# Kernel tuning notes

Measured on AMD Instinct MI355X. Metric: run time of the kernel, lower is better.

## Reference

```python
import jax, jax.numpy as jnp
import numpy as np

D_MODEL, D_FF, H, B, S = 1024, 4096, 16, 4, 2048
D_K = D_MODEL // H
EPS = 1e-5
NEG = -1e9


def _custom_ln(x, alpha, bias):
    # torch: mean, std (unbiased, N-1), alpha*(x-mean)/(std+eps)+bias; alpha/bias scalars
    mean = jnp.mean(x, axis=-1, keepdims=True)
    n = x.shape[-1]
    var = jnp.sum((x - mean) ** 2, axis=-1, keepdims=True) / (n - 1)
    std = jnp.sqrt(var)
    return alpha * (x - mean) / (std + EPS) + bias


def setup_inputs() -> dict:
    key = jax.random.key(0)
    ks = jax.random.split(key, 12)
    sc_d = 1.0 / np.sqrt(D_MODEL)
    sc_f = 1.0 / np.sqrt(D_FF)
    inp = {
        "x": jax.random.normal(ks[0], (B, S, D_MODEL), jnp.float32),
        "src_mask": jnp.ones((B, 1, 1, S), jnp.int32),
        "wq": jax.random.normal(ks[1], (D_MODEL, D_MODEL), jnp.float32) * sc_d,
        "bq": jnp.zeros((D_MODEL,), jnp.float32),
        "wk": jax.random.normal(ks[2], (D_MODEL, D_MODEL), jnp.float32) * sc_d,
        "bk": jnp.zeros((D_MODEL,), jnp.float32),
        "wv": jax.random.normal(ks[3], (D_MODEL, D_MODEL), jnp.float32) * sc_d,
        "bv": jnp.zeros((D_MODEL,), jnp.float32),
        "wo": jax.random.normal(ks[4], (D_MODEL, D_MODEL), jnp.float32) * sc_d,
        "bo": jnp.zeros((D_MODEL,), jnp.float32),
        "w1": jax.random.normal(ks[5], (D_MODEL, D_FF), jnp.float32) * sc_d,
        "b1": jnp.zeros((D_FF,), jnp.float32),
        "w2": jax.random.normal(ks[6], (D_FF, D_MODEL), jnp.float32) * sc_f,
        "b2": jnp.zeros((D_MODEL,), jnp.float32),
        "ln1_a": jnp.ones((1,), jnp.float32),
        "ln1_b": jnp.zeros((1,), jnp.float32),
        "ln2_a": jnp.ones((1,), jnp.float32),
        "ln2_b": jnp.zeros((1,), jnp.float32),
    }
    return inp


def _attention(xn, src_mask, wq, bq, wk, bk, wv, bv, wo, bo):
    q = (xn @ wq + bq).reshape(B, S, H, D_K).transpose(0, 2, 1, 3)  # [B,H,S,Dk]
    k = (xn @ wk + bk).reshape(B, S, H, D_K).transpose(0, 2, 1, 3)
    v = (xn @ wv + bv).reshape(B, S, H, D_K).transpose(0, 2, 1, 3)
    scores = jnp.einsum("bhqd,bhkd->bhqk", q, k) / np.sqrt(D_K)
    scores = jnp.where(src_mask == 0, NEG, scores)
    attn = jax.nn.softmax(scores, axis=-1)
    ctx = jnp.einsum("bhqk,bhkd->bhqd", attn, v)
    ctx = ctx.transpose(0, 2, 1, 3).reshape(B, S, D_MODEL)
    return ctx @ wo + bo


def reference(x, src_mask, wq, bq, wk, bk, wv, bv, wo, bo,
              w1, b1, w2, b2, ln1_a, ln1_b, ln2_a, ln2_b):
    # pre-LN attention residual (dropout=0 -> identity)
    xn = _custom_ln(x, ln1_a, ln1_b)
    x = x + _attention(xn, src_mask, wq, bq, wk, bk, wv, bv, wo, bo)
    # pre-LN FFN residual
    xn = _custom_ln(x, ln2_a, ln2_b)
    ff = jax.nn.relu(xn @ w1 + b1) @ w2 + b2
    return x + ff
```

## Files before the change

kernel.cpp:

```cpp
#include <hip/hip_runtime.h>

typedef unsigned short u16;
typedef __bf16 bf16x8 __attribute__((ext_vector_type(8)));
typedef float f32x4 __attribute__((ext_vector_type(4)));

__device__ __forceinline__ u16 f2bf(float f) {
  unsigned u = __builtin_bit_cast(unsigned, f);
  unsigned lsb = (u >> 16) & 1u;
  u += 0x7fffu + lsb;
  return (u16)(u >> 16);
}

__device__ __forceinline__ unsigned cvt_pk_bf16(float lo, float hi) {
  unsigned r;
  asm("v_cvt_pk_bf16_f32 %0, %1, %2" : "=v"(r) : "v"(lo), "v"(hi));
  return r;
}

__device__ __forceinline__ void gld_lds16(const u16* g, u16* l) {
  __builtin_amdgcn_global_load_lds(
      (__attribute__((address_space(1))) void*)g,
      (__attribute__((address_space(3))) void*)l, 16, 0, 0);
}

__global__ __launch_bounds__(256) void ln_kernel(
    const float* __restrict__ x, u16* __restrict__ out,
    const float* __restrict__ alpha_p, const float* __restrict__ beta_p) {
  const int row = blockIdx.x;
  const int t = threadIdx.x;
  const float4 v = reinterpret_cast<const float4*>(x + (size_t)row * 1024)[t];
  float s = v.x + v.y + v.z + v.w;
  float sq = v.x * v.x + v.y * v.y + v.z * v.z + v.w * v.w;
#pragma unroll
  for (int off = 32; off > 0; off >>= 1) {
    s += __shfl_down(s, off);
    sq += __shfl_down(sq, off);
  }
  __shared__ float red[8];
  const int w = t >> 6;
  if ((t & 63) == 0) { red[w] = s; red[4 + w] = sq; }
  __syncthreads();
  const float ts = red[0] + red[1] + red[2] + red[3];
  const float tq = red[4] + red[5] + red[6] + red[7];
  const float mean = ts * (1.0f / 1024.0f);
  float var = (tq - ts * mean) * (1.0f / 1023.0f);
  var = fmaxf(var, 0.0f);
  const float rden = 1.0f / (sqrtf(var) + 1e-5f);
  const float a = alpha_p[0], bb = beta_p[0];
  uint2 ov;
  ov.x = cvt_pk_bf16(a * (v.x - mean) * rden + bb, a * (v.y - mean) * rden + bb);
  ov.y = cvt_pk_bf16(a * (v.z - mean) * rden + bb, a * (v.w - mean) * rden + bb);
  reinterpret_cast<uint2*>(out + (size_t)row * 1024)[t] = ov;
}

__global__ __launch_bounds__(256) void wcvt_t(
    const float* __restrict__ w, u16* __restrict__ wt, int K, int N, float scale) {
  __shared__ float tile[32][33];
  const int n0 = blockIdx.x * 32, k0 = blockIdx.y * 32;
  const int tx = threadIdx.x, ty = threadIdx.y;
#pragma unroll
  for (int i = 0; i < 4; ++i)
    tile[ty + i * 8][tx] = w[(size_t)(k0 + ty + i * 8) * N + n0 + tx];
  __syncthreads();
#pragma unroll
  for (int i = 0; i < 4; ++i)
    wt[(size_t)(n0 + ty + i * 8) * K + k0 + tx] = f2bf(tile[tx][ty + i * 8] * scale);
}

__global__ __launch_bounds__(256) void pack_bias(
    const float* __restrict__ a, const float* __restrict__ b,
    const float* __restrict__ c, float* __restrict__ o, float qscale) {
  const int i = blockIdx.x * 256 + threadIdx.x;
  o[i] = (i < 1024) ? a[i] * qscale : ((i < 2048) ? b[i - 1024] : c[i - 2048]);
}

__global__ __launch_bounds__(256) void mk_mbias(
    const int* __restrict__ mask, float* __restrict__ mb, int* __restrict__ flags) {
  const int b = blockIdx.x, t = threadIdx.x;
  __shared__ int bad;
  if (t == 0) bad = 0;
  __syncthreads();
  int loc = 0;
#pragma unroll
  for (int i = 0; i < 8; ++i) {
    const int idx = b * 2048 + t * 8 + i;
    const int mv = mask[idx];
    mb[idx] = mv ? 0.f : -1.4427e9f;
    loc |= (mv == 0);
  }
  if (loc) atomicOr(&bad, 1);
  __syncthreads();
  if (t == 0) flags[b] = !bad;
}

template <int EPI, int BM>
__global__ __launch_bounds__(512, BM == 256 ? 2 : 4) void gemm8(
    const u16* __restrict__ A, const u16* __restrict__ Bt,
    const float* __restrict__ bias, const float* __restrict__ res,
    void* __restrict__ Cout, u16* __restrict__ vt, int M, int N, int K) {
  constexpr int MF = BM / 32;
  constexpr int NA = (BM == 256) ? 2 : 1;
  extern __shared__ u16 smem[];
  u16* Asb = smem;
  u16* Bsb = smem + 3 * BM * 32;

  const int tid = threadIdx.x;
  const int l = tid & 63;
  const int w = tid >> 6;
  const int wr = w >> 2, wc = w & 3;
  const int gx = gridDim.x;
  int id = blockIdx.y * gx + blockIdx.x;
  const int nwg = gx * gridDim.y;
  id = (id & 7) * (nwg >> 3) + (id >> 3);
  const int n0 = (id % gx) * 256;
  const int m0 = (id / gx) * BM;
  const int lr = l & 15, lg = l >> 4;
  const int koff = (lg ^ ((lr >> 1) & 3)) * 8;

  f32x4 acc[MF][4];
#pragma unroll
  for (int i = 0; i < MF; ++i)
#pragma unroll
    for (int j = 0; j < 4; ++j) acc[i][j] = f32x4{0.f, 0.f, 0.f, 0.f};

  const u16* aSrc[NA];
  int aOff[NA];
#pragma unroll
  for (int i = 0; i < NA; ++i) {
    const int ci = tid + i * 512;
    const int row = ci >> 2, c = ci & 3;
    const int sc = c ^ ((row >> 1) & 3);
    aSrc[i] = A + (size_t)(m0 + row) * K + sc * 8;
    aOff[i] = ci * 8;
  }
  const u16* bSrc[2];
  int bOff[2];
#pragma unroll
  for (int i = 0; i < 2; ++i) {
    const int ci = tid + i * 512;
    const int row = ci >> 2, c = ci & 3;
    const int sc = c ^ ((row >> 1) & 3);
    bSrc[i] = Bt + (size_t)(n0 + row) * K + sc * 8;
    bOff[i] = ci * 8;
  }

  const int NT = K >> 5;
#pragma unroll
  for (int i = 0; i < NA; ++i) gld_lds16(aSrc[i], Asb + aOff[i]);
#pragma unroll
  for (int i = 0; i < 2; ++i) gld_lds16(bSrc[i], Bsb + bOff[i]);
#pragma unroll
  for (int i = 0; i < NA; ++i) gld_lds16(aSrc[i] + 32, Asb + BM * 32 + aOff[i]);
#pragma unroll
  for (int i = 0; i < 2; ++i) gld_lds16(bSrc[i] + 32, Bsb + 256 * 32 + bOff[i]);
  if constexpr (NA == 2) asm volatile("s_waitcnt vmcnt(4)" ::: "memory");
  else asm volatile("s_waitcnt vmcnt(3)" ::: "memory");
  __builtin_amdgcn_s_barrier();

  int cur = 0;
  for (int t = 0; t < NT; ++t) {
    const int nx2 = (cur + 2 >= 3) ? cur - 1 : cur + 2;
    if (t + 2 < NT) {
      const int ko = (t + 2) * 32;
#pragma unroll
      for (int i = 0; i < NA; ++i) gld_lds16(aSrc[i] + ko, Asb + nx2 * BM * 32 + aOff[i]);
#pragma unroll
      for (int i = 0; i < 2; ++i) gld_lds16(bSrc[i] + ko, Bsb + nx2 * 256 * 32 + bOff[i]);
    }
    const u16* Ab = Asb + cur * BM * 32;
    const u16* Bb = Bsb + cur * 256 * 32;
    bf16x8 a[MF], b[4];
#pragma unroll
    for (int mf = 0; mf < MF; ++mf)
      a[mf] = *reinterpret_cast<const bf16x8*>(&Ab[(wr * (BM / 2) + mf * 16 + lr) * 32 + koff]);
#pragma unroll
    for (int nf = 0; nf < 4; ++nf)
      b[nf] = *reinterpret_cast<const bf16x8*>(&Bb[(wc * 64 + nf * 16 + lr) * 32 + koff]);
    __builtin_amdgcn_s_setprio(1);
#pragma unroll
    for (int mf = 0; mf < MF; ++mf)
#pragma unroll
      for (int nf = 0; nf < 4; ++nf)
        acc[mf][nf] = __builtin_amdgcn_mfma_f32_16x16x32_bf16(a[mf], b[nf], acc[mf][nf], 0, 0, 0);
    __builtin_amdgcn_s_setprio(0);
    if (t + 2 < NT) {
      if constexpr (NA == 2) asm volatile("s_waitcnt vmcnt(4)" ::: "memory");
      else asm volatile("s_waitcnt vmcnt(3)" ::: "memory");
    } else {
      asm volatile("s_waitcnt vmcnt(0)" ::: "memory");
    }
    __builtin_amdgcn_s_barrier();
    cur = (cur + 1 >= 3) ? 0 : cur + 1;
  }

  if (EPI == 3 && n0 >= 2048) {
#pragma unroll
    for (int mf = 0; mf < MF; ++mf) {
#pragma unroll
      for (int nf = 0; nf < 4; ++nf) {
        const int col = n0 + wc * 64 + nf * 16 + lr;
        const float bv = bias[col];
        const int row0 = m0 + wr * (BM / 2) + mf * 16 + lg * 4;
        const int bb = row0 >> 11, s0 = row0 & 2047;
        const int d = col - 2048;
        uint2 pv;
        pv.x = cvt_pk_bf16(acc[mf][nf][0] + bv, acc[mf][nf][1] + bv);
        pv.y = cvt_pk_bf16(acc[mf][nf][2] + bv, acc[mf][nf][3] + bv);
        *reinterpret_cast<uint2*>(vt + ((size_t)bb * 1024 + d) * 2048 + s0) = pv;
      }
    }
    return;
  }

#pragma unroll
  for (int mf = 0; mf < MF; ++mf) {
#pragma unroll
    for (int nf = 0; nf < 4; ++nf) {
      const int col = n0 + wc * 64 + nf * 16 + lr;
      const float bv = bias[col];
#pragma unroll
      for (int j = 0; j < 4; ++j) {
        const int row = m0 + wr * (BM / 2) + mf * 16 + lg * 4 + j;
        const size_t idx = (size_t)row * N + col;
        const float vv = acc[mf][nf][j] + bv;
        if (EPI == 1)
          ((float*)Cout)[idx] = vv + res[idx];
        else if (EPI == 2)
          ((u16*)Cout)[idx] = f2bf(fmaxf(vv, 0.f));
        else
          ((u16*)Cout)[idx] = f2bf(vv);
      }
    }
  }
}

__global__ __launch_bounds__(256, 4) void attn_fwd7(
    const u16* __restrict__ qkv, const u16* __restrict__ vt,
    const float* __restrict__ mbias, const int* __restrict__ flags,
    u16* __restrict__ ctx) {
  __shared__ u16 Ks[2][64 * 64];
  __shared__ u16 Vs[2][64 * 64];
  const int tid = threadIdx.x;
  const int l = tid & 63;
  const int w = tid >> 6;
  const int p = blockIdx.y * 16 + blockIdx.x;
  const int idx = p >> 3;
  const int bh = (p & 7) * 8 + (idx >> 4);
  const int qx = idx & 15;
  const int b = bh >> 4, h = bh & 15;
  const int r0 = qx * 128 + w * 32;
  const int lr = l & 15, lg = l >> 4;

  const u16* qb = qkv + (size_t)b * 2048 * 3072 + h * 64;
  const u16* kp = qb + 1024;
  const u16* vb = vt + ((size_t)b * 1024 + h * 64) * 2048;
  const float* mb = mbias + (size_t)b * 2048;
  const int allLive = flags[b];

  bf16x8 qf[2][2];
#pragma unroll
  for (int m = 0; m < 2; ++m)
#pragma unroll
    for (int ks = 0; ks < 2; ++ks)
      qf[m][ks] = *reinterpret_cast<const bf16x8*>(
          qb + (size_t)(r0 + m * 16 + lr) * 3072 + ks * 32 + lg * 8);

  bf16x8 ones;
#pragma unroll
  for (int e = 0; e < 8; ++e) ones[e] = (__bf16)1.0f;

  float mrun[2] = {-1e30f, -1e30f};
  f32x4 osum[2];
  f32x4 o[2][4];
#pragma unroll
  for (int m = 0; m < 2; ++m) {
    osum[m] = f32x4{0.f, 0.f, 0.f, 0.f};
#pragma unroll
    for (int d = 0; d < 4; ++d) o[m][d] = f32x4{0.f, 0.f, 0.f, 0.f};
  }

  const u16* kS[2];
  const u16* vS[2];
#pragma unroll
  for (int i = 0; i < 2; ++i) {
    const int ci = tid + i * 256;
    const int row = ci >> 3, cc = ci & 7;
    const int sc = cc ^ (row & 7);
    kS[i] = kp + (size_t)row * 3072 + sc * 8;
    vS[i] = vb + (size_t)row * 2048 + sc * 8;
  }
#pragma unroll
  for (int i = 0; i < 2; ++i) {
    const int ci8 = (tid + i * 256) * 8;
    gld_lds16(kS[i], &Ks[0][ci8]);
    gld_lds16(vS[i], &Vs[0][ci8]);
  }
  asm volatile("s_waitcnt vmcnt(0)" ::: "memory");
  __syncthreads();

  union U8 { unsigned u[4]; bf16x8 v; };

  int cur = 0;
  for (int t = 0; t < 32; ++t) {
    const int kb0 = t * 64;
    if (t + 1 < 32) {
      const int nb = kb0 + 64;
#pragma unroll
      for (int i = 0; i < 2; ++i) {
        const int ci8 = (tid + i * 256) * 8;
        gld_lds16(kS[i] + (size_t)nb * 3072, &Ks[cur ^ 1][ci8]);
        gld_lds16(vS[i] + nb, &Vs[cur ^ 1][ci8]);
      }
    }

    f32x4 st[2][4];
    __builtin_amdgcn_s_setprio(1);
#pragma unroll
    for (int cf = 0; cf < 4; ++cf) {
      const int krow = cf * 16 + lr;
      const int ch0 = lg ^ (krow & 7);
      const int ch1 = (4 + lg) ^ (krow & 7);
      const bf16x8 kf0 = *reinterpret_cast<const bf16x8*>(&Ks[cur][krow * 64 + ch0 * 8]);
      const bf16x8 kf1 = *reinterpret_cast<const bf16x8*>(&Ks[cur][krow * 64 + ch1 * 8]);
#pragma unroll
      for (int m = 0; m < 2; ++m) {
        f32x4 acc = __builtin_amdgcn_mfma_f32_16x16x32_bf16(kf0, qf[m][0],
                                                            f32x4{0.f, 0.f, 0.f, 0.f}, 0, 0, 0);
        st[m][cf] = __builtin_amdgcn_mfma_f32_16x16x32_bf16(kf1, qf[m][1], acc, 0, 0, 0);
      }
    }
    __builtin_amdgcn_s_setprio(0);

    if (!allLive) {
#pragma unroll
      for (int cf = 0; cf < 4; ++cf) {
        const float4 m4 = *reinterpret_cast<const float4*>(mb + kb0 + cf * 16 + lg * 4);
#pragma unroll
        for (int m = 0; m < 2; ++m) {
          st[m][cf][0] += m4.x;
          st[m][cf][1] += m4.y;
          st[m][cf][2] += m4.z;
          st[m][cf][3] += m4.w;
        }
      }
    }

    bf16x8 paA[2], paB[2];
#pragma unroll
    for (int m = 0; m < 2; ++m) {
      float p0 = fmaxf(fmaxf(st[m][0][0], st[m][0][1]), st[m][0][2]);
      float p1 = fmaxf(fmaxf(st[m][0][3], st[m][1][0]), st[m][1][1]);
      float p2 = fmaxf(fmaxf(st[m][1][2], st[m][1][3]), st[m][2][0]);
      float p3 = fmaxf(fmaxf(st[m][2][1], st[m][2][2]), st[m][2][3]);
      float p4 = fmaxf(fmaxf(st[m][3][0], st[m][3][1]), st[m][3][2]);
      float pm = fmaxf(fmaxf(p0, p1), p2);
      pm = fmaxf(fmaxf(pm, p3), p4);
      pm = fmaxf(pm, st[m][3][3]);
      pm = fmaxf(pm, __shfl_xor(pm, 16));
      pm = fmaxf(pm, __shfl_xor(pm, 32));
      if (__any(pm > mrun[m] + 8.f)) {
        const float mn = fmaxf(mrun[m], pm);
        const float corr = exp2f(mrun[m] - mn);
        mrun[m] = mn;
#pragma unroll
        for (int j = 0; j < 4; ++j) osum[m][j] *= corr;
#pragma unroll
        for (int d = 0; d < 4; ++d)
#pragma unroll
          for (int j = 0; j < 4; ++j) o[m][d][j] *= corr;
      }
#pragma unroll
      for (int cf = 0; cf < 4; ++cf)
#pragma unroll
        for (int j = 0; j < 4; ++j)
          st[m][cf][j] = exp2f(st[m][cf][j] - mrun[m]);

      unsigned pk[4][2];
#pragma unroll
      for (int cf = 0; cf < 4; ++cf)
#pragma unroll
        for (int wp = 0; wp < 2; ++wp)
          pk[cf][wp] = cvt_pk_bf16(st[m][cf][2 * wp], st[m][cf][2 * wp + 1]);

      U8 a0, a1;
#pragma unroll
      for (int c = 0; c < 2; ++c) {
        const int src = lr + 16 * ((2 * lg + c) & 3);
#pragma unroll
        for (int wp = 0; wp < 2; ++wp) {
          const int v00 = __shfl((int)pk[0][wp], src);
          const int v01 = __shfl((int)pk[1][wp], src);
          const int v10 = __shfl((int)pk[2][wp], src);
          const int v11 = __shfl((int)pk[3][wp], src);
          a0.u[2 * c + wp] = (unsigned)((lg < 2) ? v00 : v01);
          a1.u[2 * c + wp] = (unsigned)((lg < 2) ? v10 : v11);
        }
      }
      paA[m] = a0.v;
      paB[m] = a1.v;
    }

    __builtin_amdgcn_s_setprio(1);
#pragma unroll
    for (int df = 0; df < 4; ++df) {
      const int vrow = df * 16 + lr;
      const int ch0 = lg ^ (vrow & 7);
      const int ch1 = (4 + lg) ^ (vrow & 7);
      const bf16x8 vf0 = *reinterpret_cast<const bf16x8*>(&Vs[cur][vrow * 64 + ch0 * 8]);
      const bf16x8 vf1 = *reinterpret_cast<const bf16x8*>(&Vs[cur][vrow * 64 + ch1 * 8]);
#pragma unroll
      for (int m = 0; m < 2; ++m) {
        o[m][df] = __builtin_amdgcn_mfma_f32_16x16x32_bf16(vf0, paA[m], o[m][df], 0, 0, 0);
        o[m][df] = __builtin_amdgcn_mfma_f32_16x16x32_bf16(vf1, paB[m], o[m][df], 0, 0, 0);
      }
    }
#pragma unroll
    for (int m = 0; m < 2; ++m) {
      osum[m] = __builtin_amdgcn_mfma_f32_16x16x32_bf16(ones, paA[m], osum[m], 0, 0, 0);
      osum[m] = __builtin_amdgcn_mfma_f32_16x16x32_bf16(ones, paB[m], osum[m], 0, 0, 0);
    }
    __builtin_amdgcn_s_setprio(0);

    asm volatile("s_waitcnt vmcnt(0)" ::: "memory");
    __syncthreads();
    cur ^= 1;
  }

#pragma unroll
  for (int m = 0; m < 2; ++m) {
    const float rdiv = 1.f / osum[m][0];
    const size_t rowbase = ((size_t)b * 2048 + r0 + m * 16 + lr) * 1024 + h * 64;
#pragma unroll
    for (int df = 0; df < 4; ++df) {
      uint2 s4;
      s4.x = cvt_pk_bf16(o[m][df][0] * rdiv, o[m][df][1] * rdiv);
      s4.y = cvt_pk_bf16(o[m][df][2] * rdiv, o[m][df][3] * rdiv);
      *reinterpret_cast<uint2*>(ctx + rowbase + df * 16 + lg * 4) = s4;
    }
  }
}

extern "C" void kernel_launch(void* const* d_in, const int* in_sizes, int n_in,
                              void* d_out, int out_size, void* d_ws, size_t ws_size,
                              hipStream_t stream) {
  const float* x = (const float*)d_in[0];
  const int* mask = (const int*)d_in[1];
  const float* wq = (const float*)d_in[2];
  const float* bq = (const float*)d_in[3];
  const float* wk = (const float*)d_in[4];
  const float* bk = (const float*)d_in[5];
  const float* wv = (const float*)d_in[6];
  const float* bv = (const float*)d_in[7];
  const float* wo = (const float*)d_in[8];
  const float* bo = (const float*)d_in[9];
  const float* w1 = (const float*)d_in[10];
  const float* b1 = (const float*)d_in[11];
  const float* w2 = (const float*)d_in[12];
  const float* b2 = (const float*)d_in[13];
  const float* ln1a = (const float*)d_in[14];
  const float* ln1b = (const float*)d_in[15];
  const float* ln2a = (const float*)d_in[16];
  const float* ln2b = (const float*)d_in[17];

  const float SCL2 = 0.125f * 1.4426950408889634f;
  const size_t LDS256 = 3 * (256 + 256) * 32 * sizeof(u16);
  const size_t LDS128 = 3 * (128 + 256) * 32 * sizeof(u16);

  hipFuncSetAttribute((const void*)&gemm8<3, 256>,
                      hipFuncAttributeMaxDynamicSharedMemorySize, (int)LDS256);
  hipFuncSetAttribute((const void*)&gemm8<2, 256>,
                      hipFuncAttributeMaxDynamicSharedMemorySize, (int)LDS256);
  hipFuncSetAttribute((const void*)&gemm8<1, 128>,
                      hipFuncAttributeMaxDynamicSharedMemorySize, (int)LDS128);

  char* ws = (char*)d_ws;
  const size_t MB = 1024ull * 1024ull;
  u16* WTQKV = (u16*)(ws + 0 * MB);
  u16* WTO = (u16*)(ws + 6 * MB);
  u16* W1T = (u16*)(ws + 8 * MB);
  u16* W2T = (u16*)(ws + 16 * MB);
  float* BQKV = (float*)(ws + 24 * MB);
  float* MBIAS = (float*)(ws + 24 * MB + 65536);
  int* FLAGS = (int*)(ws + 24 * MB + 131072);
  u16* QKV = (u16*)(ws + 25 * MB);
  u16* VT = (u16*)(ws + 73 * MB);
  u16* XN = (u16*)(ws + 89 * MB);
  u16* CTX = (u16*)(ws + 105 * MB);
  float* X2 = (float*)(ws + 25 * MB);
  u16* XN2 = (u16*)(ws + 57 * MB);
  u16* H1 = (u16*)(ws + 73 * MB);

  dim3 bt(32, 8);
  wcvt_t<<<dim3(32, 32), bt, 0, stream>>>(wq, WTQKV, 1024, 1024, SCL2);
  wcvt_t<<<dim3(32, 32), bt, 0, stream>>>(wk, WTQKV + 1024 * 1024, 1024, 1024, 1.f);
  wcvt_t<<<dim3(32, 32), bt, 0, stream>>>(wv, WTQKV + 2048 * 1024, 1024, 1024, 1.f);
  wcvt_t<<<dim3(32, 32), bt, 0, stream>>>(wo, WTO, 1024, 1024, 1.f);
  wcvt_t<<<dim3(128, 32), bt, 0, stream>>>(w1, W1T, 1024, 4096, 1.f);
  wcvt_t<<<dim3(32, 128), bt, 0, stream>>>(w2, W2T, 4096, 1024, 1.f);
  pack_bias<<<dim3(12), 256, 0, stream>>>(bq, bk, bv, BQKV, SCL2);
  mk_mbias<<<dim3(4), 256, 0, stream>>>(mask, MBIAS, FLAGS);

  ln_kernel<<<8192, 256, 0, stream>>>(x, XN, ln1a, ln1b);
  gemm8<3, 256><<<dim3(12, 32), 512, LDS256, stream>>>(XN, WTQKV, BQKV, nullptr, QKV, VT, 8192, 3072, 1024);
  attn_fwd7<<<dim3(16, 64), 256, 0, stream>>>(QKV, VT, MBIAS, FLAGS, CTX);
  gemm8<1, 128><<<dim3(4, 64), 512, LDS128, stream>>>(CTX, WTO, bo, x, X2, nullptr, 8192, 1024, 1024);
  ln_kernel<<<8192, 256, 0, stream>>>(X2, XN2, ln2a, ln2b);
  gemm8<2, 256><<<dim3(16, 32), 512, LDS256, stream>>>(XN2, W1T, b1, nullptr, H1, nullptr, 8192, 4096, 1024);
  gemm8<1, 128><<<dim3(4, 64), 512, LDS128, stream>>>(H1, W2T, b2, X2, (float*)d_out, nullptr, 8192, 1024, 4096);
}
```

Baseline: 455.4 us.

## Triple-buffer attention K/V tiles with one barrier per iteration

The attention kernel moves from double to triple-buffered K/V LDS tiles, prefetching two tiles ahead. It uses a partial vmcnt wait and a single barrier at the top of each iteration instead of a full drain plus barrier at the end. It also swaps __shfl for ds_bpermute with precomputed byte offsets. The larger LDS footprint lowers the occupancy hint from 4 to 3 blocks per CU, trading latency hiding from occupancy for latency hiding from deeper prefetch.

```diff
diff --git a/kernel.cpp b/kernel.cpp
--- a/kernel.cpp
+++ b/kernel.cpp
@@ -234,12 +234,12 @@
   }
 }
 
-__global__ __launch_bounds__(256, 4) void attn_fwd7(
+__global__ __launch_bounds__(256, 3) void attn_fwd8(
     const u16* __restrict__ qkv, const u16* __restrict__ vt,
     const float* __restrict__ mbias, const int* __restrict__ flags,
     u16* __restrict__ ctx) {
-  __shared__ u16 Ks[2][64 * 64];
-  __shared__ u16 Vs[2][64 * 64];
+  __shared__ u16 Ks[3][64 * 64];
+  __shared__ u16 Vs[3][64 * 64];
   const int tid = threadIdx.x;
   const int l = tid & 63;
   const int w = tid >> 6;
@@ -279,6 +279,9 @@
     for (int d = 0; d < 4; ++d) o[m][d] = f32x4{0.f, 0.f, 0.f, 0.f};
   }
 
+  const int srcb0 = (lr + 16 * ((2 * lg + 0) & 3)) << 2;
+  const int srcb1 = (lr + 16 * ((2 * lg + 1) & 3)) << 2;
+
   const u16* kS[2];
   const u16* vS[2];
 #pragma unroll
@@ -295,23 +298,31 @@
     gld_lds16(kS[i], &Ks[0][ci8]);
     gld_lds16(vS[i], &Vs[0][ci8]);
   }
-  asm volatile("s_waitcnt vmcnt(0)" ::: "memory");
-  __syncthreads();
+#pragma unroll
+  for (int i = 0; i < 2; ++i) {
+    const int ci8 = (tid + i * 256) * 8;
+    gld_lds16(kS[i] + (size_t)64 * 3072, &Ks[1][ci8]);
+    gld_lds16(vS[i] + 64, &Vs[1][ci8]);
+  }
 
   union U8 { unsigned u[4]; bf16x8 v; };
 
   int cur = 0;
   for (int t = 0; t < 32; ++t) {
-    const int kb0 = t * 64;
-    if (t + 1 < 32) {
-      const int nb = kb0 + 64;
+    if (t < 31) asm volatile("s_waitcnt vmcnt(4)" ::: "memory");
+    else asm volatile("s_waitcnt vmcnt(0)" ::: "memory");
+    __builtin_amdgcn_s_barrier();
+    if (t + 2 < 32) {
+      const int nx2 = (cur + 2 >= 3) ? cur - 1 : cur + 2;
+      const int nb = (t + 2) * 64;
 #pragma unroll
       for (int i = 0; i < 2; ++i) {
         const int ci8 = (tid + i * 256) * 8;
-        gld_lds16(kS[i] + (size_t)nb * 3072, &Ks[cur ^ 1][ci8]);
-        gld_lds16(vS[i] + nb, &Vs[cur ^ 1][ci8]);
-      }
-    }
+        gld_lds16(kS[i] + (size_t)nb * 3072, &Ks[nx2][ci8]);
+        gld_lds16(vS[i] + nb, &Vs[nx2][ci8]);
+      }
+    }
+    const int kb0 = t * 64;
 
     f32x4 st[2][4];
     __builtin_amdgcn_s_setprio(1);
@@ -385,13 +396,13 @@
       U8 a0, a1;
 #pragma unroll
       for (int c = 0; c < 2; ++c) {
-        const int src = lr + 16 * ((2 * lg + c) & 3);
+        const int srcb = c ? srcb1 : srcb0;
 #pragma unroll
         for (int wp = 0; wp < 2; ++wp) {
-          const int v00 = __shfl((int)pk[0][wp], src);
-          const int v01 = __shfl((int)pk[1][wp], src);
-          const int v10 = __shfl((int)pk[2][wp], src);
-          const int v11 = __shfl((int)pk[3][wp], src);
+          const int v00 = __builtin_amdgcn_ds_bpermute(srcb, (int)pk[0][wp]);
+          const int v01 = __builtin_amdgcn_ds_bpermute(srcb, (int)pk[1][wp]);
+          const int v10 = __builtin_amdgcn_ds_bpermute(srcb, (int)pk[2][wp]);
+          const int v11 = __builtin_amdgcn_ds_bpermute(srcb, (int)pk[3][wp]);
           a0.u[2 * c + wp] = (unsigned)((lg < 2) ? v00 : v01);
           a1.u[2 * c + wp] = (unsigned)((lg < 2) ? v10 : v11);
         }
@@ -421,9 +432,7 @@
     }
     __builtin_amdgcn_s_setprio(0);
 
-    asm volatile("s_waitcnt vmcnt(0)" ::: "memory");
-    __syncthreads();
-    cur ^= 1;
+    cur = (cur + 1 >= 3) ? 0 : cur + 1;
   }
 
 #pragma unroll
@@ -502,7 +511,7 @@
 
   ln_kernel<<<8192, 256, 0, stream>>>(x, XN, ln1a, ln1b);
   gemm8<3, 256><<<dim3(12, 32), 512, LDS256, stream>>>(XN, WTQKV, BQKV, nullptr, QKV, VT, 8192, 3072, 1024);
-  attn_fwd7<<<dim3(16, 64), 256, 0, stream>>>(QKV, VT, MBIAS, FLAGS, CTX);
+  attn_fwd8<<<dim3(16, 64), 256, 0, stream>>>(QKV, VT, MBIAS, FLAGS, CTX);
   gemm8<1, 128><<<dim3(4, 64), 512, LDS128, stream>>>(CTX, WTO, bo, x, X2, nullptr, 8192, 1024, 1024);
   ln_kernel<<<8192, 256, 0, stream>>>(X2, XN2, ln2a, ln2b);
   gemm8<2, 256><<<dim3(16, 32), 512, LDS256, stream>>>(XN2, W1T, b1, nullptr, H1, nullptr, 8192, 4096, 1024);
```

After: 468.6 us. 1.03x slower.
